# Kernel tuning notes

Hardware: AMD Instinct MI355X
Metric: run time of the kernel (lower is better)

The kernel has to match this reference:

```python
import jax, jax.numpy as jnp
from jax import lax
import numpy as np

# Model hyperparameters (match init_kwargs)
NUM_STEPS = 6
N_ETYPES = 8
D_IN = 128
D_OUT = 128
B, N, E = 32, 1024, 262144  # graphs, nodes per graph, total edges


def setup_inputs() -> dict:
    key = jax.random.key(0)
    ks = jax.random.split(key, 24)
    s = 0.05  # param scale for numeric stability over 6 GRU steps
    inp = {
        "h": jax.random.normal(ks[0], (B, N, D_IN), jnp.float32),
        "src": jax.random.randint(ks[1], (E,), 0, B * N, jnp.int32),
        "dst": jax.random.randint(ks[2], (E,), 0, B * N, jnp.int32),
        "etype": jax.random.randint(ks[3], (E,), 0, N_ETYPES, jnp.int32),
        "W_msg": jax.random.normal(ks[4], (N_ETYPES, D_OUT, D_OUT), jnp.float32) * s,
        "b_msg": jax.random.normal(ks[5], (N_ETYPES, D_OUT), jnp.float32) * s,
        "w_ih": jax.random.normal(ks[6], (3 * D_OUT, D_OUT), jnp.float32) * s,
        "w_hh": jax.random.normal(ks[7], (3 * D_OUT, D_OUT), jnp.float32) * s,
        "b_ih": jax.random.normal(ks[8], (3 * D_OUT,), jnp.float32) * s,
        "b_hh": jax.random.normal(ks[9], (3 * D_OUT,), jnp.float32) * s,
        "conv1_w": jax.random.normal(ks[10], (D_OUT, D_OUT, 3), jnp.float32) * s,
        "conv1_b": jax.random.normal(ks[11], (D_OUT,), jnp.float32) * s,
        "conv2_w": jax.random.normal(ks[12], (D_OUT, D_OUT, 1), jnp.float32) * s,
        "conv2_b": jax.random.normal(ks[13], (D_OUT,), jnp.float32) * s,
        "cc1_w": jax.random.normal(ks[14], (D_IN + D_OUT, D_IN + D_OUT, 3), jnp.float32) * s,
        "cc1_b": jax.random.normal(ks[15], (D_IN + D_OUT,), jnp.float32) * s,
        "cc2_w": jax.random.normal(ks[16], (D_IN + D_OUT, D_IN + D_OUT, 1), jnp.float32) * s,
        "cc2_b": jax.random.normal(ks[17], (D_IN + D_OUT,), jnp.float32) * s,
        "mlp_y_w": jax.random.normal(ks[18], (1, D_OUT), jnp.float32) * s,
        "mlp_y_b": jax.random.normal(ks[19], (1,), jnp.float32) * s,
        "mlp_z_w": jax.random.normal(ks[20], (1, D_IN + D_OUT), jnp.float32) * s,
        "mlp_z_b": jax.random.normal(ks[21], (1,), jnp.float32) * s,
    }
    return inp


def _conv1d(x, w, b):
    # x: [B, C_in, L], w: [C_out, C_in, K]
    y = lax.conv_general_dilated(x, w, (1,), "VALID",
                                 dimension_numbers=("NCW", "OIW", "NCW"))
    return y + b[None, :, None]


def _maxpool1d(x, k, stride):
    return lax.reduce_window(x, -jnp.inf, lax.max,
                             (1, 1, k), (1, 1, stride), "VALID")


def _ggnn(h0, src, dst, etype, W_msg, b_msg, w_ih, w_hh, b_ih, b_hh):
    # h0: [BN, D_OUT] (in_feats == out_feats so no zero-padding needed)
    n_nodes = h0.shape[0]

    def step(h, _):
        # transform each node by every etype weight: [BN, T, O]
        t = jnp.einsum("nd,tod->nto", h, W_msg) + b_msg
        m = t[src, etype]                                   # [E, O] gather
        a = jax.ops.segment_sum(m, dst, num_segments=n_nodes)  # scatter-add
        # torch.nn.GRUCell(a, h)
        gi = a @ w_ih.T + b_ih
        gh = h @ w_hh.T + b_hh
        i_r, i_z, i_n = jnp.split(gi, 3, axis=-1)
        h_r, h_z, h_n = jnp.split(gh, 3, axis=-1)
        r = jax.nn.sigmoid(i_r + h_r)
        z = jax.nn.sigmoid(i_z + h_z)
        n = jnp.tanh(i_n + r * h_n)
        return (1.0 - z) * n + z * h, None

    h_final, _ = lax.scan(step, h0, None, length=NUM_STEPS)
    return h_final


def reference(h, src, dst, etype, W_msg, b_msg, w_ih, w_hh, b_ih, b_hh,
              conv1_w, conv1_b, conv2_w, conv2_b, cc1_w, cc1_b, cc2_w, cc2_b,
              mlp_y_w, mlp_y_b, mlp_z_w, mlp_z_b):
    b, n, d = h.shape
    x = h.reshape(b * n, d)
    h_next = _ggnn(x, src, dst, etype, W_msg, b_msg, w_ih, w_hh, b_ih, b_hh)
    h_i = h_next.reshape(b, n, -1)                   # [B, N, O]
    c_i = jnp.concatenate([h_i, h], axis=-1)          # [B, N, O+D]

    Y_1 = _maxpool1d(jax.nn.relu(_conv1d(h_i.transpose(0, 2, 1), conv1_w, conv1_b)), 3, 2)
    Y_2 = _maxpool1d(jax.nn.relu(_conv1d(Y_1, conv2_w, conv2_b)), 2, 2).transpose(0, 2, 1)
    Z_1 = _maxpool1d(jax.nn.relu(_conv1d(c_i.transpose(0, 2, 1), cc1_w, cc1_b)), 3, 2)
    Z_2 = _maxpool1d(jax.nn.relu(_conv1d(Z_1, cc2_w, cc2_b)), 2, 2).transpose(0, 2, 1)

    before_avg = (Y_2 @ mlp_y_w.T + mlp_y_b) * (Z_2 @ mlp_z_w.T + mlp_z_b)  # [B, L, 1]
    avg = before_avg.mean(axis=1)                     # [B, 1]
    return jax.nn.sigmoid(avg).squeeze(-1)            # [B]
```

## Files before the change

kernel.cpp:

```cpp
#include <hip/hip_runtime.h>
#include <math.h>

#define BB 32
#define NNODE 1024
#define BN 32768
#define NE 262144
#define DD 128
#define NT 8
#define NSTEPS 6
#define NBIN 16
#define SORT_CAP (NE + 2048)
#define NTILES_F 2064
#define M_CAP (NE + 2048)

typedef __attribute__((ext_vector_type(8))) short bf16x8;
typedef __attribute__((ext_vector_type(4))) float f32x4;

static __device__ __forceinline__ float4 ld4(const float* p) { return *(const float4*)p; }
static __device__ __forceinline__ float sigmoidf_(float x) { return 1.f / (1.f + expf(-x)); }
static __device__ __forceinline__ unsigned f2b(float f) {
    unsigned u = __float_as_uint(f);
    return (u + 0x7FFFu + ((u >> 16) & 1u)) >> 16;
}
static __device__ __forceinline__ float b2f(unsigned short b) {
    return __uint_as_float(((unsigned)b) << 16);
}
static __device__ __forceinline__ unsigned pk(float a, float b) {
    return f2b(a) | (f2b(b) << 16);
}
static __device__ __forceinline__ unsigned bmax2(unsigned a, unsigned b) {
    unsigned ah = a & 0xFFFF0000u, bh = b & 0xFFFF0000u;
    unsigned al = a & 0x0000FFFFu, bl = b & 0x0000FFFFu;
    return (ah > bh ? ah : bh) | (al > bl ? al : bl);
}
static __device__ __forceinline__ uint4 bmax4(uint4 a, uint4 b) {
    return make_uint4(bmax2(a.x, b.x), bmax2(a.y, b.y), bmax2(a.z, b.z), bmax2(a.w, b.w));
}

static constexpr size_t OFF_HCUR = 0;
static constexpr size_t OFF_HBF  = OFF_HCUR + (size_t)BN * DD * 4;
static constexpr size_t OFF_CNT  = OFF_HBF  + (size_t)BN * DD * 2;
static constexpr size_t OFF_DOFF = OFF_CNT  + (size_t)BN * NT * 4;
static constexpr size_t OFF_DBLK = OFF_DOFF + (size_t)BN * 4;
static constexpr size_t OFF_HB   = OFF_DBLK + 512;
static constexpr size_t OFF_SSRC = OFF_HB   + 256;
static constexpr size_t OFF_SDST = OFF_SSRC + (size_t)SORT_CAP * 4;
static constexpr size_t OFF_SQ   = OFF_SDST + (size_t)SORT_CAP * 4;
static constexpr size_t OFF_DCUR = OFF_SQ   + (size_t)SORT_CAP * 4;
static constexpr size_t OFF_DEG  = OFF_DCUR + (size_t)BN * 4;
static constexpr size_t OFF_WMB  = OFF_DEG  + (size_t)BN * 4;
static constexpr size_t OFF_WIHB = OFF_WMB  + (size_t)NT * DD * DD * 2;
static constexpr size_t OFF_WHHB = OFF_WIHB + (size_t)3 * DD * DD * 2;
static constexpr size_t OFF_W1PY = OFF_WHHB + (size_t)3 * DD * DD * 2;
static constexpr size_t OFF_W1PZ = OFF_W1PY + (size_t)3 * 128 * 128 * 2;
static constexpr size_t OFF_W2YB = OFF_W1PZ + (size_t)3 * 256 * 256 * 2;
static constexpr size_t OFF_W2ZB = OFF_W2YB + (size_t)128 * 128 * 2;
static constexpr size_t OFF_ABF  = OFF_W2ZB + (size_t)256 * 256 * 2;
static constexpr size_t OFF_H0BF = OFF_ABF  + (size_t)BN * DD * 2;
static constexpr size_t OFF_UN   = OFF_H0BF + (size_t)BN * DD * 2;
static constexpr size_t OFF_M    = OFF_UN;
static constexpr size_t OFF_U1Y  = OFF_UN;
static constexpr size_t OFF_U1Z  = OFF_U1Y + (size_t)32 * 1024 * 128 * 2;
static constexpr size_t OFF_QY   = OFF_U1Z + (size_t)32 * 1024 * 256 * 2;
static constexpr size_t OFF_QZ   = OFF_QY  + (size_t)32 * 255 * 128 * 4;
static constexpr size_t CONV_SZ  = (size_t)32 * 1024 * 128 * 2 + (size_t)32 * 1024 * 256 * 2
                                 + (size_t)32 * 255 * 128 * 4 + (size_t)32 * 255 * 256 * 4;
static constexpr size_t M_SZ     = (size_t)M_CAP * 128 * 2;
static constexpr size_t UN_SZ    = (M_SZ > CONV_SZ ? M_SZ : CONV_SZ);
static constexpr size_t WS_NEED  = OFF_UN + UN_SZ;

#define PREP_BLOCKS 6133
__global__ void k_prep(const float* __restrict__ h_in, float* __restrict__ hcur,
                       unsigned short* __restrict__ hbf, unsigned short* __restrict__ h0bf,
                       const float* __restrict__ Wmsg, unsigned short* __restrict__ wmb,
                       const float* __restrict__ wih, unsigned short* __restrict__ wihb,
                       const float* __restrict__ whh, unsigned short* __restrict__ whhb,
                       const float* __restrict__ c2w, unsigned short* __restrict__ w2yb,
                       const float* __restrict__ z2w, unsigned short* __restrict__ w2zb,
                       const float* __restrict__ c1w, unsigned short* __restrict__ w1py,
                       const float* __restrict__ z1w, unsigned short* __restrict__ w1pz,
                       int* __restrict__ cnt, int* __restrict__ hb,
                       int* __restrict__ ssrc, int* __restrict__ sdst)
{
    int blk = blockIdx.x, tid = threadIdx.x;
    if (blk < 4096) {
        int i = blk * 256 + tid;
        float4 v = ((const float4*)h_in)[i];
        ((float4*)hcur)[i] = v;
        uint2 p = make_uint2(pk(v.x, v.y), pk(v.z, v.w));
        ((uint2*)hbf)[i] = p;
        ((uint2*)h0bf)[i] = p;
    } else if (blk < 4224) {
        int i = (blk - 4096) * 256 + tid;
        float4 v = ((const float4*)Wmsg)[i];
        ((uint2*)wmb)[i] = make_uint2(pk(v.x, v.y), pk(v.z, v.w));
    } else if (blk < 4272) {
        int i = (blk - 4224) * 256 + tid;
        float4 v = ((const float4*)wih)[i];
        ((uint2*)wihb)[i] = make_uint2(pk(v.x, v.y), pk(v.z, v.w));
    } else if (blk < 4320) {
        int i = (blk - 4272) * 256 + tid;
        float4 v = ((const float4*)whh)[i];
        ((uint2*)whhb)[i] = make_uint2(pk(v.x, v.y), pk(v.z, v.w));
    } else if (blk < 4336) {
        int i = (blk - 4320) * 256 + tid;
        float4 v = ((const float4*)c2w)[i];
        ((uint2*)w2yb)[i] = make_uint2(pk(v.x, v.y), pk(v.z, v.w));
    } else if (blk < 4400) {
        int i = (blk - 4336) * 256 + tid;
        float4 v = ((const float4*)z2w)[i];
        ((uint2*)w2zb)[i] = make_uint2(pk(v.x, v.y), pk(v.z, v.w));
    } else if (blk < 4592) {
        int g = (blk - 4400) * 256 + tid;
        int k = g >> 14, rem = g & 16383;
        w1py[g] = (unsigned short)f2b(c1w[(size_t)rem * 3 + k]);
    } else if (blk < 5360) {
        int g = (blk - 4592) * 256 + tid;
        int k = g >> 16, rem = g & 65535;
        w1pz[g] = (unsigned short)f2b(z1w[(size_t)rem * 3 + k]);
    } else if (blk < 5616) {
        ((uint4*)cnt)[(blk - 5360) * 256 + tid] = make_uint4(0, 0, 0, 0);
    } else if (blk < 5617) {
        if (tid < 64) hb[tid] = 0;
    } else if (blk < 5875) {
        ((uint4*)ssrc)[(blk - 5617) * 256 + tid] = make_uint4(0, 0, 0, 0);
    } else {
        ((uint4*)sdst)[(blk - 5875) * 256 + tid] = make_uint4(~0u, ~0u, ~0u, ~0u);
    }
}


__global__ void k_hist(const int* __restrict__ et, const int* __restrict__ dst,
                       int* __restrict__ hb, int* __restrict__ cnt)
{
    __shared__ int lh[NBIN];
    int tid = threadIdx.x;
    if (tid < NBIN) lh[tid] = 0;
    __syncthreads();
    int base = blockIdx.x * 1024;
    for (int k = 0; k < 4; ++k) {
        int e = base + tid + k * 256;
        int t = et[e], d = dst[e];
        atomicAdd(&lh[((d >> 14) << 3) | t], 1);
        atomicAdd(&cnt[d * NT + t], 1);
    }
    __syncthreads();
    if (tid < NBIN) atomicAdd(&hb[tid], lh[tid]);
}

__global__ void k_degA(const int* __restrict__ cnt, int* __restrict__ deg,
                       int* __restrict__ doff, int* __restrict__ dblk)
{
    __shared__ int ps[256];
    int tid = threadIdx.x;
    int v = blockIdx.x * 256 + tid;
    const int* cv = cnt + (size_t)v * NT;
    int d = 0;
#pragma unroll
    for (int t = 0; t < NT; ++t) d += cv[t];
    deg[v] = d;
    ps[tid] = d;
    __syncthreads();
    for (int off = 1; off < 256; off <<= 1) {
        int x = 0;
        if (tid >= off) x = ps[tid - off];
        __syncthreads();
        ps[tid] += x;
        __syncthreads();
    }
    doff[v] = ps[tid] - d;
    if (tid == 255) dblk[blockIdx.x] = ps[255];
}

__global__ void k_scan2(int* __restrict__ hb, int* __restrict__ dblk)
{
    __shared__ int s[128];
    int tid = threadIdx.x;
    s[tid] = dblk[tid];
    __syncthreads();
    if (tid == 0) {
        int acc = 0;
        for (int t = 0; t < NBIN; ++t) {
            hb[16 + t] = acc;
            hb[33 + t] = acc;
            acc += ((hb[t] + 127) >> 7) << 7;
        }
        hb[32] = acc;
        int run = 0;
        for (int i = 0; i < 128; ++i) {
            int x = s[i]; s[i] = run; run += x;
        }
    }
    __syncthreads();
    dblk[tid] = s[tid];
}

__global__ void k_degB(int* __restrict__ doff, int* __restrict__ dcur,
                       const int* __restrict__ dblk)
{
    int v = blockIdx.x * 256 + threadIdx.x;
    int o = doff[v] + dblk[blockIdx.x];
    doff[v] = o;
    dcur[v] = o;
}

__global__ void k_scatter(const int* __restrict__ src, const int* __restrict__ dst,
                          const int* __restrict__ et, int* __restrict__ hb,
                          int* __restrict__ dcur,
                          int* __restrict__ ssrc, int* __restrict__ sdst, int* __restrict__ sq)
{
    __shared__ int lc[NBIN], lbase[NBIN];
    int tid = threadIdx.x;
    if (tid < NBIN) lc[tid] = 0;
    __syncthreads();
    int base = blockIdx.x * 1024;
    int myk[4], myr[4];
    for (int k = 0; k < 4; ++k) {
        int e = base + tid * 4 + k;
        int kk = ((dst[e] >> 14) << 3) | et[e];
        myk[k] = kk;
        myr[k] = atomicAdd(&lc[kk], 1);
    }
    __syncthreads();
    if (tid < NBIN) lbase[tid] = atomicAdd(&hb[33 + tid], lc[tid]);
    __syncthreads();
    for (int k = 0; k < 4; ++k) {
        int e = base + tid * 4 + k;
        int p = lbase[myk[k]] + myr[k];
        int d = dst[e];
        ssrc[p] = src[e];
        sdst[p] = d;
        sq[p] = atomicAdd(&dcur[d], 1);
    }
}


__launch_bounds__(256, 3)
__global__ void k_msg(const int* __restrict__ ssrc, const int* __restrict__ sdst,
                      const int* __restrict__ sq, const int* __restrict__ hb,
                      const unsigned short* __restrict__ hbf,
                      const unsigned short* __restrict__ wmb,
                      unsigned short* __restrict__ m)
{
    __shared__ __align__(16) unsigned short As[128 * 64];
    __shared__ __align__(16) unsigned short Ws[128 * 64];
    __shared__ int sdl[128], ssl[128], sql[128];
    int base = blockIdx.x * 128;
    if (base >= hb[32]) return;
    int bin = 0;
#pragma unroll
    for (int i = 1; i < NBIN; ++i) if (base >= hb[16 + i]) bin = i;
    int t = bin & 7;
    int tid = threadIdx.x;
    if (tid < 128) { sdl[tid] = sdst[base + tid]; ssl[tid] = ssrc[base + tid]; sql[tid] = sq[base + tid]; }
    __syncthreads();
    int lane = tid & 63, wvv = tid >> 6;
    int wm = (wvv >> 1) * 64, wn = (wvv & 1) * 64;
    int lr = lane & 15, lk = lane >> 4;
    f32x4 acc[4][4];
#pragma unroll
    for (int i = 0; i < 4; ++i)
#pragma unroll
        for (int j = 0; j < 4; ++j) acc[i][j] = (f32x4){0.f, 0.f, 0.f, 0.f};

    int r = tid >> 1, halfc = tid & 1;
    unsigned boff = r * 128 + halfc * 64;
    unsigned sw = (r & 7) << 4;
    for (int c0 = 0; c0 < DD; c0 += 64) {
        if (c0) __syncthreads();
        {
            const uint4* hp = (const uint4*)(hbf + (size_t)ssl[r] * DD + c0 + halfc * 32);
            const uint4* wp = (const uint4*)(wmb + (size_t)t * DD * DD + (size_t)r * DD + c0 + halfc * 32);
#pragma unroll
            for (int c = 0; c < 4; ++c) {
                unsigned byte = (boff + c * 16) ^ sw;
                *(uint4*)((char*)As + byte) = hp[c];
                *(uint4*)((char*)Ws + byte) = wp[c];
            }
        }
        __syncthreads();
#pragma unroll
        for (int kc = 0; kc < 2; ++kc) {
            int cb = kc * 64 + lk * 16;
            bf16x8 af[4], bfv[4];
#pragma unroll
            for (int mi = 0; mi < 4; ++mi) {
                int row = wm + mi * 16 + lr;
                af[mi] = *(const bf16x8*)((const char*)As + ((row * 128 + cb) ^ ((row & 7) << 4)));
            }
#pragma unroll
            for (int ni = 0; ni < 4; ++ni) {
                int row = wn + ni * 16 + lr;
                bfv[ni] = *(const bf16x8*)((const char*)Ws + ((row * 128 + cb) ^ ((row & 7) << 4)));
            }
#pragma unroll
            for (int mi = 0; mi < 4; ++mi)
#pragma unroll
                for (int ni = 0; ni < 4; ++ni)
                    acc[mi][ni] = __builtin_amdgcn_mfma_f32_16x16x32_bf16(af[mi], bfv[ni], acc[mi][ni], 0, 0, 0);
        }
    }
    __syncthreads();
    {
        unsigned short* tgt = wn ? Ws : As;
#pragma unroll
        for (int mi = 0; mi < 4; ++mi)
#pragma unroll
            for (int ni = 0; ni < 4; ++ni)
#pragma unroll
                for (int rg = 0; rg < 4; ++rg) {
                    int er = wm + mi * 16 + lk * 4 + rg;
                    int col = (wn + ni * 16 + lr) & 63;
                    unsigned byte = ((unsigned)(er * 128 + col * 2)) ^ ((er & 7) << 4);
                    *(unsigned short*)((char*)tgt + byte) = (unsigned short)f2b(acc[mi][ni][rg]);
                }
    }
    __syncthreads();
    int orow = tid >> 4, ochunk = tid & 15;
#pragma unroll
    for (int p = 0; p < 8; ++p) {
        int row = p * 16 + orow;
        if (sdl[row] >= 0) {
            const char* srcb = (ochunk < 8) ? (const char*)As : (const char*)Ws;
            unsigned byte = ((unsigned)(row * 128 + (ochunk & 7) * 16)) ^ ((row & 7) << 4);
            uint4 v = *(const uint4*)(srcb + byte);
            *(uint4*)(m + (size_t)sql[row] * 128 + ochunk * 8) = v;
        }
    }
}


__launch_bounds__(256)
__global__ void k_agg(const unsigned short* __restrict__ m, const int* __restrict__ deg,
                      const int* __restrict__ doff, const int* __restrict__ cnt,
                      const float* __restrict__ bmsg, unsigned short* __restrict__ abf)
{
    __shared__ float bm[NT * DD];
    int tid = threadIdx.x;
    *(float4*)&bm[tid * 4] = ld4(bmsg + tid * 4);
    __syncthreads();
    int wv = tid >> 6, lane = tid & 63;
    int v = blockIdx.x * 4 + wv;
    int lh = lane >> 5;
    int lc = lane & 31;
    float a0 = 0.f, a1 = 0.f, a2 = 0.f, a3 = 0.f;
    if (lh == 0) {
        const int* cv = cnt + (size_t)v * NT;
        int c0 = lc * 4;
#pragma unroll
        for (int t = 0; t < NT; ++t) {
            float c = (float)cv[t];
            a0 += c * bm[t * DD + c0];
            a1 += c * bm[t * DD + c0 + 1];
            a2 += c * bm[t * DD + c0 + 2];
            a3 += c * bm[t * DD + c0 + 3];
        }
    }
    int d = deg[v], off = doff[v];
    const uint2* mr = (const uint2*)m;
    int npair = d >> 1;
    for (int i = 0; i < npair; ++i) {
        uint2 w = mr[(size_t)(off + 2 * i + lh) * 32 + lc];
        a0 += b2f((unsigned short)(w.x & 0xFFFF));
        a1 += b2f((unsigned short)(w.x >> 16));
        a2 += b2f((unsigned short)(w.y & 0xFFFF));
        a3 += b2f((unsigned short)(w.y >> 16));
    }
    if ((d & 1) && lh == 0) {
        uint2 w = mr[(size_t)(off + d - 1) * 32 + lc];
        a0 += b2f((unsigned short)(w.x & 0xFFFF));
        a1 += b2f((unsigned short)(w.x >> 16));
        a2 += b2f((unsigned short)(w.y & 0xFFFF));
        a3 += b2f((unsigned short)(w.y >> 16));
    }
    a0 += __shfl_xor(a0, 32);
    a1 += __shfl_xor(a1, 32);
    a2 += __shfl_xor(a2, 32);
    a3 += __shfl_xor(a3, 32);
    if (lh == 0)
        ((uint2*)abf)[(size_t)v * 32 + lc] = make_uint2(pk(a0, a1), pk(a2, a3));
}


__launch_bounds__(512, 2)
__global__ void k_gru(const unsigned short* __restrict__ abf, float* __restrict__ h,
                      unsigned short* __restrict__ hbf,
                      const unsigned short* __restrict__ wihb, const unsigned short* __restrict__ whhb,
                      const float* __restrict__ bih, const float* __restrict__ bhh)
{
    __shared__ __align__(16) unsigned short Xs[128 * 128];
    __shared__ __align__(16) unsigned short Ws2[128 * 128];
    int m0 = blockIdx.x * 128;
    int tid = threadIdx.x;
    int lane = tid & 63, wv = tid >> 6;
    int wm = (wv >> 1) * 32, wn = (wv & 1) * 64;
    int lr = lane & 15, lk = lane >> 4;
    f32x4 aR[2][4], aZ[2][4], aI[2][4], aH[2][4];
#pragma unroll
    for (int i = 0; i < 2; ++i)
#pragma unroll
        for (int j = 0; j < 4; ++j) {
            aR[i][j] = (f32x4){0.f, 0.f, 0.f, 0.f};
            aZ[i][j] = (f32x4){0.f, 0.f, 0.f, 0.f};
            aI[i][j] = (f32x4){0.f, 0.f, 0.f, 0.f};
            aH[i][j] = (f32x4){0.f, 0.f, 0.f, 0.f};
        }
    int rx = tid >> 2, qx = tid & 3;
    unsigned bx = rx * 256 + qx * 64, swx = (rx & 7) << 4;
#pragma unroll
    for (int pass = 0; pass < 2; ++pass) {
        const unsigned short* X = pass ? hbf : abf;
        const unsigned short* W = pass ? whhb : wihb;
#pragma unroll
        for (int g = 0; g < 3; ++g) {
            __syncthreads();
            if (g == 0) {
                const uint4* sp = (const uint4*)(X + (size_t)(m0 + rx) * DD + qx * 32);
#pragma unroll
                for (int c = 0; c < 4; ++c)
                    *(uint4*)((char*)Xs + ((bx + c * 16) ^ swx)) = sp[c];
            }
            {
                const uint4* wp = (const uint4*)(W + (size_t)(g * DD + rx) * DD + qx * 32);
#pragma unroll
                for (int c = 0; c < 4; ++c)
                    *(uint4*)((char*)Ws2 + ((bx + c * 16) ^ swx)) = wp[c];
            }
            __syncthreads();
#pragma unroll
            for (int kc = 0; kc < 4; ++kc) {
                int cb = kc * 64 + lk * 16;
                bf16x8 af[2], bfv[4];
#pragma unroll
                for (int mi = 0; mi < 2; ++mi) {
                    int row = wm + mi * 16 + lr;
                    af[mi] = *(const bf16x8*)((const char*)Xs + ((row * 256 + cb) ^ ((row & 7) << 4)));
                }
#pragma unroll
                for (int ni = 0; ni < 4; ++ni) {
                    int row = wn + ni * 16 + lr;
                    bfv[ni] = *(const bf16x8*)((const char*)Ws2 + ((row * 256 + cb) ^ ((row & 7) << 4)));
                }
#pragma unroll
                for (int mi = 0; mi < 2; ++mi)
#pragma unroll
                    for (int ni = 0; ni < 4; ++ni) {
                        if (g == 0)
                            aR[mi][ni] = __builtin_amdgcn_mfma_f32_16x16x32_bf16(af[mi], bfv[ni], aR[mi][ni], 0, 0, 0);
                        else if (g == 1)
                            aZ[mi][ni] = __builtin_amdgcn_mfma_f32_16x16x32_bf16(af[mi], bfv[ni], aZ[mi][ni], 0, 0, 0);
                        else if (pass == 0)
                            aI[mi][ni] = __builtin_amdgcn_mfma_f32_16x16x32_bf16(af[mi], bfv[ni], aI[mi][ni], 0, 0, 0);
                        else
                            aH[mi][ni] = __builtin_amdgcn_mfma_f32_16x16x32_bf16(af[mi], bfv[ni], aH[mi][ni], 0, 0, 0);
                    }
            }
        }
    }
#pragma unroll
    for (int ni = 0; ni < 4; ++ni) {
        int col = wn + ni * 16 + lr;
        float br_ = bih[col] + bhh[col];
        float bz_ = bih[DD + col] + bhh[DD + col];
        float bin_ = bih[2 * DD + col], bhn_ = bhh[2 * DD + col];
#pragma unroll
        for (int mi = 0; mi < 2; ++mi)
#pragma unroll
            for (int rg = 0; rg < 4; ++rg) {
                int v = m0 + wm + mi * 16 + lk * 4 + rg;
                float rr = sigmoidf_(aR[mi][ni][rg] + br_);
                float zz = sigmoidf_(aZ[mi][ni][rg] + bz_);
                float nn = tanhf(aI[mi][ni][rg] + bin_ + rr * (aH[mi][ni][rg] + bhn_));
                float hold = h[(size_t)v * DD + col];
                float hnew = (1.f - zz) * nn + zz * hold;
                h[(size_t)v * DD + col] = hnew;
                hbf[(size_t)v * DD + col] = (unsigned short)f2b(hnew);
            }
    }
}


template <int CIN>
__launch_bounds__(256, 2)
__global__ void k_conv1m(const unsigned short* __restrict__ hbf, const unsigned short* __restrict__ h0bf,
                         const unsigned short* __restrict__ w1p, const float* __restrict__ bias,
                         unsigned short* __restrict__ U1)
{
    __shared__ __align__(16) unsigned short As[128 * 64];
    __shared__ __align__(16) unsigned short Ws[128 * 64];
    int p0 = blockIdx.x * 128, b = blockIdx.y, n0 = blockIdx.z * 128;
    int tid = threadIdx.x;
    int lane = tid & 63, wv = tid >> 6;
    int wm = (wv >> 1) * 64, wn = (wv & 1) * 64;
    int lr = lane & 15, lk = lane >> 4;
    f32x4 acc[4][4];
#pragma unroll
    for (int i = 0; i < 4; ++i)
#pragma unroll
        for (int j = 0; j < 4; ++j) acc[i][j] = (f32x4){0.f, 0.f, 0.f, 0.f};

    int r = tid >> 1, halfc = tid & 1;
    unsigned boff = r * 128 + halfc * 64;
    unsigned sw = (r & 7) << 4;
#pragma unroll
    for (int k = 0; k < 3; ++k) {
        for (int c0 = 0; c0 < CIN; c0 += 64) {
            __syncthreads();
            {
                int row = p0 + k + r; if (row > NNODE - 1) row = NNODE - 1;
                int ci = c0 + halfc * 32;
                const unsigned short* srcp = (CIN == 128 || ci < 128)
                    ? hbf  + ((size_t)(b * NNODE + row)) * DD + ci
                    : h0bf + ((size_t)(b * NNODE + row)) * DD + (ci - 128);
                const uint4* sp = (const uint4*)srcp;
#pragma unroll
                for (int c = 0; c < 4; ++c)
                    *(uint4*)((char*)As + ((boff + c * 16) ^ sw)) = sp[c];
            }
            {
                const uint4* wp = (const uint4*)(w1p + ((size_t)k * CIN + n0 + r) * CIN + c0 + halfc * 32);
#pragma unroll
                for (int c = 0; c < 4; ++c)
                    *(uint4*)((char*)Ws + ((boff + c * 16) ^ sw)) = wp[c];
            }
            __syncthreads();
#pragma unroll
            for (int kc = 0; kc < 2; ++kc) {
                int cb = kc * 64 + lk * 16;
                bf16x8 af[4], bfv[4];
#pragma unroll
                for (int mi = 0; mi < 4; ++mi) {
                    int row = wm + mi * 16 + lr;
                    af[mi] = *(const bf16x8*)((const char*)As + ((row * 128 + cb) ^ ((row & 7) << 4)));
                }
#pragma unroll
                for (int ni = 0; ni < 4; ++ni) {
                    int row = wn + ni * 16 + lr;
                    bfv[ni] = *(const bf16x8*)((const char*)Ws + ((row * 128 + cb) ^ ((row & 7) << 4)));
                }
#pragma unroll
                for (int mi = 0; mi < 4; ++mi)
#pragma unroll
                    for (int ni = 0; ni < 4; ++ni)
                        acc[mi][ni] = __builtin_amdgcn_mfma_f32_16x16x32_bf16(af[mi], bfv[ni], acc[mi][ni], 0, 0, 0);
            }
        }
    }
#pragma unroll
    for (int ni = 0; ni < 4; ++ni) {
        int co = n0 + wn + ni * 16 + lr;
        float bs = bias[co];
#pragma unroll
        for (int mi = 0; mi < 4; ++mi)
#pragma unroll
            for (int rg = 0; rg < 4; ++rg) {
                int pos = p0 + wm + mi * 16 + lk * 4 + rg;
                if (pos < NNODE - 2) {
                    float v = fmaxf(0.f, acc[mi][ni][rg] + bs);
                    U1[((size_t)b * NNODE + pos) * CIN + co] = (unsigned short)f2b(v);
                }
            }
    }
}


template <int CIN>
__launch_bounds__(256, 2)
__global__ void k_conv2m(const unsigned short* __restrict__ U1, const unsigned short* __restrict__ w2b,
                         const float* __restrict__ bias, float* __restrict__ Q)
{
    __shared__ __align__(16) unsigned short As[128 * 64];
    __shared__ __align__(16) unsigned short Ws[128 * 64];
    int m0 = blockIdx.x * 128, b = blockIdx.y, n0 = blockIdx.z * 128;
    int tid = threadIdx.x;
    int lane = tid & 63, wv = tid >> 6;
    int wm = (wv >> 1) * 64, wn = (wv & 1) * 64;
    int lr = lane & 15, lk = lane >> 4;
    f32x4 acc[4][4];
#pragma unroll
    for (int i = 0; i < 4; ++i)
#pragma unroll
        for (int j = 0; j < 4; ++j) acc[i][j] = (f32x4){0.f, 0.f, 0.f, 0.f};

    int r = tid >> 1, halfc = tid & 1;
    unsigned boff = r * 128 + halfc * 64;
    unsigned sw = (r & 7) << 4;
    for (int c0 = 0; c0 < CIN; c0 += 64) {
        __syncthreads();
        {
            int pr = 2 * (m0 + r);
            int r0 = pr, r1 = pr + 1, r2v = pr + 2;
            if (r2v > NNODE - 1) r2v = NNODE - 1;
            if (r1 > NNODE - 1) r1 = NNODE - 1;
            int ci = c0 + halfc * 32;
            const unsigned short* bp = U1 + (size_t)b * NNODE * CIN + ci;
            const uint4* p0q = (const uint4*)(bp + (size_t)r0 * CIN);
            const uint4* p1q = (const uint4*)(bp + (size_t)r1 * CIN);
            const uint4* p2q = (const uint4*)(bp + (size_t)r2v * CIN);
#pragma unroll
            for (int c = 0; c < 4; ++c) {
                uint4 mm = bmax4(bmax4(p0q[c], p1q[c]), p2q[c]);
                *(uint4*)((char*)As + ((boff + c * 16) ^ sw)) = mm;
            }
        }
        {
            const uint4* wp = (const uint4*)(w2b + (size_t)(n0 + r) * CIN + c0 + halfc * 32);
#pragma unroll
            for (int c = 0; c < 4; ++c)
                *(uint4*)((char*)Ws + ((boff + c * 16) ^ sw)) = wp[c];
        }
        __syncthreads();
#pragma unroll
        for (int kc = 0; kc < 2; ++kc) {
            int cb = kc * 64 + lk * 16;
            bf16x8 af[4], bfv[4];
#pragma unroll
            for (int mi = 0; mi < 4; ++mi) {
                int row = wm + mi * 16 + lr;
                af[mi] = *(const bf16x8*)((const char*)As + ((row * 128 + cb) ^ ((row & 7) << 4)));
            }
#pragma unroll
            for (int ni = 0; ni < 4; ++ni) {
                int row = wn + ni * 16 + lr;
                bfv[ni] = *(const bf16x8*)((const char*)Ws + ((row * 128 + cb) ^ ((row & 7) << 4)));
            }
#pragma unroll
            for (int mi = 0; mi < 4; ++mi)
#pragma unroll
                for (int ni = 0; ni < 4; ++ni)
                    acc[mi][ni] = __builtin_amdgcn_mfma_f32_16x16x32_bf16(af[mi], bfv[ni], acc[mi][ni], 0, 0, 0);
        }
    }
#pragma unroll
    for (int ni = 0; ni < 4; ++ni) {
        int co = n0 + wn + ni * 16 + lr;
        float bs = bias[co];
#pragma unroll
        for (int mi = 0; mi < 4; ++mi) {
            int l0 = m0 + wm + mi * 16 + lk * 4;
            float v0 = fmaxf(0.f, acc[mi][ni][0] + bs);
            float v1 = fmaxf(0.f, acc[mi][ni][1] + bs);
            float v2 = fmaxf(0.f, acc[mi][ni][2] + bs);
            float v3 = fmaxf(0.f, acc[mi][ni][3] + bs);
            int jq = l0 >> 1;
            if (jq < 255)     Q[((size_t)b * 255 + jq) * CIN + co]     = fmaxf(v0, v1);
            if (jq + 1 < 255) Q[((size_t)b * 255 + jq + 1) * CIN + co] = fmaxf(v2, v3);
        }
    }
}


__launch_bounds__(256)
__global__ void k_final(const float* __restrict__ QY, const float* __restrict__ QZ,
                        const float* __restrict__ wy, const float* __restrict__ by,
                        const float* __restrict__ wz, const float* __restrict__ bz,
                        float* __restrict__ out)
{
    int b = blockIdx.x, tid = threadIdx.x;
    float p = 0.f;
    if (tid < 255) {
        const float* qy = QY + ((size_t)(b * 255 + tid)) * 128;
        const float* qz = QZ + ((size_t)(b * 255 + tid)) * 256;
        float dy = 0.f, dz = 0.f;
        for (int c = 0; c < 128; c += 4) {
            float4 q = ld4(qy + c), wv = ld4(wy + c);
            dy += q.x * wv.x + q.y * wv.y + q.z * wv.z + q.w * wv.w;
        }
        for (int c = 0; c < 256; c += 4) {
            float4 q = ld4(qz + c), wv = ld4(wz + c);
            dz += q.x * wv.x + q.y * wv.y + q.z * wv.z + q.w * wv.w;
        }
        p = (dy + by[0]) * (dz + bz[0]);
    }
    __shared__ float red[4];
    for (int off = 32; off > 0; off >>= 1) p += __shfl_down(p, off);
    if ((tid & 63) == 0) red[tid >> 6] = p;
    __syncthreads();
    if (tid == 0) {
        float s = red[0] + red[1] + red[2] + red[3];
        out[b] = 1.f / (1.f + expf(-s / 255.f));
    }
}


extern "C" void kernel_launch(void* const* d_in, const int* in_sizes, int n_in,
                              void* d_out, int out_size, void* d_ws, size_t ws_size,
                              hipStream_t stream)
{
    const float* h_in = (const float*)d_in[0];
    const int* src = (const int*)d_in[1];
    const int* dst = (const int*)d_in[2];
    const int* et  = (const int*)d_in[3];
    const float* Wmsg = (const float*)d_in[4];
    const float* bmsg = (const float*)d_in[5];
    const float* wih = (const float*)d_in[6];
    const float* whh = (const float*)d_in[7];
    const float* bih = (const float*)d_in[8];
    const float* bhh = (const float*)d_in[9];
    const float* c1w = (const float*)d_in[10];
    const float* c1b = (const float*)d_in[11];
    const float* c2w = (const float*)d_in[12];
    const float* c2b = (const float*)d_in[13];
    const float* z1w = (const float*)d_in[14];
    const float* z1b = (const float*)d_in[15];
    const float* z2w = (const float*)d_in[16];
    const float* z2b = (const float*)d_in[17];
    const float* wy  = (const float*)d_in[18];
    const float* by  = (const float*)d_in[19];
    const float* wz  = (const float*)d_in[20];
    const float* bz  = (const float*)d_in[21];
    float* out = (float*)d_out;

    if (ws_size < WS_NEED) return;

    char* ws = (char*)d_ws;
    float* hcur = (float*)(ws + OFF_HCUR);
    unsigned short* hbf  = (unsigned short*)(ws + OFF_HBF);
    int*   cnt  = (int*)(ws + OFF_CNT);
    int*   doff = (int*)(ws + OFF_DOFF);
    int*   dblk = (int*)(ws + OFF_DBLK);
    int*   hb   = (int*)(ws + OFF_HB);
    int*   ssrc = (int*)(ws + OFF_SSRC);
    int*   sdst = (int*)(ws + OFF_SDST);
    int*   sq   = (int*)(ws + OFF_SQ);
    int*   dcur = (int*)(ws + OFF_DCUR);
    int*   deg  = (int*)(ws + OFF_DEG);
    unsigned short* wmb  = (unsigned short*)(ws + OFF_WMB);
    unsigned short* wihb = (unsigned short*)(ws + OFF_WIHB);
    unsigned short* whhb = (unsigned short*)(ws + OFF_WHHB);
    unsigned short* w1py = (unsigned short*)(ws + OFF_W1PY);
    unsigned short* w1pz = (unsigned short*)(ws + OFF_W1PZ);
    unsigned short* w2yb = (unsigned short*)(ws + OFF_W2YB);
    unsigned short* w2zb = (unsigned short*)(ws + OFF_W2ZB);
    unsigned short* abf  = (unsigned short*)(ws + OFF_ABF);
    unsigned short* h0bf = (unsigned short*)(ws + OFF_H0BF);
    unsigned short* mbuf = (unsigned short*)(ws + OFF_M);
    unsigned short* U1Y  = (unsigned short*)(ws + OFF_U1Y);
    unsigned short* U1Z  = (unsigned short*)(ws + OFF_U1Z);
    float* QY   = (float*)(ws + OFF_QY);
    float* QZ   = (float*)(ws + OFF_QZ);

    k_prep<<<PREP_BLOCKS, 256, 0, stream>>>(h_in, hcur, hbf, h0bf, Wmsg, wmb, wih, wihb, whh, whhb,
                                            c2w, w2yb, z2w, w2zb, c1w, w1py, z1w, w1pz,
                                            cnt, hb, ssrc, sdst);

    k_hist<<<256, 256, 0, stream>>>(et, dst, hb, cnt);
    k_degA<<<128, 256, 0, stream>>>(cnt, deg, doff, dblk);
    k_scan2<<<1, 128, 0, stream>>>(hb, dblk);
    k_degB<<<128, 256, 0, stream>>>(doff, dcur, dblk);
    k_scatter<<<256, 256, 0, stream>>>(src, dst, et, hb, dcur, ssrc, sdst, sq);

    for (int s = 0; s < NSTEPS; ++s) {
        k_msg<<<NTILES_F, 256, 0, stream>>>(ssrc, sdst, sq, hb, hbf, wmb, mbuf);
        k_agg<<<BN / 4, 256, 0, stream>>>(mbuf, deg, doff, cnt, bmsg, abf);
        k_gru<<<BN / 128, 512, 0, stream>>>(abf, hcur, hbf, wihb, whhb, bih, bhh);
    }

    k_conv1m<128><<<dim3(8, 32, 1), 256, 0, stream>>>(hbf, h0bf, w1py, c1b, U1Y);
    k_conv2m<128><<<dim3(4, 32, 1), 256, 0, stream>>>(U1Y, w2yb, c2b, QY);
    k_conv1m<256><<<dim3(8, 32, 2), 256, 0, stream>>>(hbf, h0bf, w1pz, z1b, U1Z);
    k_conv2m<256><<<dim3(4, 32, 2), 256, 0, stream>>>(U1Z, w2zb, z2b, QZ);
    k_final<<<32, 256, 0, stream>>>(QY, QZ, wy, by, wz, bz, out);
}
```

Baseline: 558.1 us.

## Fuse message aggregation into GRU kernel and raise k_msg occupancy bound

```diff
diff --git a/kernel.cpp b/kernel.cpp
--- a/kernel.cpp
+++ b/kernel.cpp
@@ -35,6 +35,16 @@
 }
 static __device__ __forceinline__ uint4 bmax4(uint4 a, uint4 b) {
     return make_uint4(bmax2(a.x, b.x), bmax2(a.y, b.y), bmax2(a.z, b.z), bmax2(a.w, b.w));
+}
+static __device__ __forceinline__ void upacc(float* ac, uint4 w0, uint4 w1) {
+    ac[0] += b2f((unsigned short)(w0.x & 0xFFFF)); ac[1] += b2f((unsigned short)(w0.x >> 16));
+    ac[2] += b2f((unsigned short)(w0.y & 0xFFFF)); ac[3] += b2f((unsigned short)(w0.y >> 16));
+    ac[4] += b2f((unsigned short)(w0.z & 0xFFFF)); ac[5] += b2f((unsigned short)(w0.z >> 16));
+    ac[6] += b2f((unsigned short)(w0.w & 0xFFFF)); ac[7] += b2f((unsigned short)(w0.w >> 16));
+    ac[8] += b2f((unsigned short)(w1.x & 0xFFFF)); ac[9] += b2f((unsigned short)(w1.x >> 16));
+    ac[10] += b2f((unsigned short)(w1.y & 0xFFFF)); ac[11] += b2f((unsigned short)(w1.y >> 16));
+    ac[12] += b2f((unsigned short)(w1.z & 0xFFFF)); ac[13] += b2f((unsigned short)(w1.z >> 16));
+    ac[14] += b2f((unsigned short)(w1.w & 0xFFFF)); ac[15] += b2f((unsigned short)(w1.w >> 16));
 }
 
 static constexpr size_t OFF_HCUR = 0;
@@ -235,7 +245,7 @@
 }
 
 
-__launch_bounds__(256, 3)
+__launch_bounds__(256, 4)
 __global__ void k_msg(const int* __restrict__ ssrc, const int* __restrict__ sdst,
                       const int* __restrict__ sq, const int* __restrict__ hb,
                       const unsigned short* __restrict__ hbf,
@@ -330,68 +340,55 @@
 }
 
 
-__launch_bounds__(256)
-__global__ void k_agg(const unsigned short* __restrict__ m, const int* __restrict__ deg,
-                      const int* __restrict__ doff, const int* __restrict__ cnt,
-                      const float* __restrict__ bmsg, unsigned short* __restrict__ abf)
-{
-    __shared__ float bm[NT * DD];
+__launch_bounds__(512, 2)
+__global__ void k_gruagg(const unsigned short* __restrict__ m, const int* __restrict__ deg,
+                         const int* __restrict__ doff, const int* __restrict__ cnt,
+                         const float* __restrict__ bmsg,
+                         float* __restrict__ h, unsigned short* __restrict__ hbf,
+                         const unsigned short* __restrict__ wihb, const unsigned short* __restrict__ whhb,
+                         const float* __restrict__ bih, const float* __restrict__ bhh)
+{
+    __shared__ __align__(16) unsigned short Xs[128 * 128];
+    __shared__ __align__(16) unsigned short Ws2[128 * 128];
+    __shared__ float bmS[NT * DD];
+    int m0 = blockIdx.x * 128;
     int tid = threadIdx.x;
-    *(float4*)&bm[tid * 4] = ld4(bmsg + tid * 4);
-    __syncthreads();
-    int wv = tid >> 6, lane = tid & 63;
-    int v = blockIdx.x * 4 + wv;
-    int lh = lane >> 5;
-    int lc = lane & 31;
-    float a0 = 0.f, a1 = 0.f, a2 = 0.f, a3 = 0.f;
-    if (lh == 0) {
-        const int* cv = cnt + (size_t)v * NT;
-        int c0 = lc * 4;
+    ((float2*)bmS)[tid] = ((const float2*)bmsg)[tid];
+
+    int rx = tid >> 2, qx = tid & 3;
+    unsigned bx = rx * 256 + qx * 64, swx = (rx & 7) << 4;
+    int v = m0 + rx;
+    int d = deg[v], off = doff[v];
+    int cv[NT];
+    {
+        uint4 c0 = *(const uint4*)(cnt + (size_t)v * NT);
+        uint4 c1 = *(const uint4*)(cnt + (size_t)v * NT + 4);
+        cv[0] = c0.x; cv[1] = c0.y; cv[2] = c0.z; cv[3] = c0.w;
+        cv[4] = c1.x; cv[5] = c1.y; cv[6] = c1.z; cv[7] = c1.w;
+    }
+    __syncthreads();
+#pragma unroll
+    for (int half = 0; half < 2; ++half) {
+        float ac[16];
+#pragma unroll
+        for (int j = 0; j < 16; ++j) ac[j] = 0.f;
 #pragma unroll
         for (int t = 0; t < NT; ++t) {
             float c = (float)cv[t];
-            a0 += c * bm[t * DD + c0];
-            a1 += c * bm[t * DD + c0 + 1];
-            a2 += c * bm[t * DD + c0 + 2];
-            a3 += c * bm[t * DD + c0 + 3];
-        }
-    }
-    int d = deg[v], off = doff[v];
-    const uint2* mr = (const uint2*)m;
-    int npair = d >> 1;
-    for (int i = 0; i < npair; ++i) {
-        uint2 w = mr[(size_t)(off + 2 * i + lh) * 32 + lc];
-        a0 += b2f((unsigned short)(w.x & 0xFFFF));
-        a1 += b2f((unsigned short)(w.x >> 16));
-        a2 += b2f((unsigned short)(w.y & 0xFFFF));
-        a3 += b2f((unsigned short)(w.y >> 16));
-    }
-    if ((d & 1) && lh == 0) {
-        uint2 w = mr[(size_t)(off + d - 1) * 32 + lc];
-        a0 += b2f((unsigned short)(w.x & 0xFFFF));
-        a1 += b2f((unsigned short)(w.x >> 16));
-        a2 += b2f((unsigned short)(w.y & 0xFFFF));
-        a3 += b2f((unsigned short)(w.y >> 16));
-    }
-    a0 += __shfl_xor(a0, 32);
-    a1 += __shfl_xor(a1, 32);
-    a2 += __shfl_xor(a2, 32);
-    a3 += __shfl_xor(a3, 32);
-    if (lh == 0)
-        ((uint2*)abf)[(size_t)v * 32 + lc] = make_uint2(pk(a0, a1), pk(a2, a3));
-}
-
-
-__launch_bounds__(512, 2)
-__global__ void k_gru(const unsigned short* __restrict__ abf, float* __restrict__ h,
-                      unsigned short* __restrict__ hbf,
-                      const unsigned short* __restrict__ wihb, const unsigned short* __restrict__ whhb,
-                      const float* __restrict__ bih, const float* __restrict__ bhh)
-{
-    __shared__ __align__(16) unsigned short Xs[128 * 128];
-    __shared__ __align__(16) unsigned short Ws2[128 * 128];
-    int m0 = blockIdx.x * 128;
-    int tid = threadIdx.x;
+            const float* bp = &bmS[t * DD + qx * 32 + half * 16];
+#pragma unroll
+            for (int j = 0; j < 16; ++j) ac[j] += c * bp[j];
+        }
+        for (int e = 0; e < d; ++e) {
+            const uint4* pp = (const uint4*)(m + ((size_t)(off + e)) * DD + qx * 32 + half * 16);
+            upacc(ac, pp[0], pp[1]);
+        }
+        uint4 o0 = make_uint4(pk(ac[0], ac[1]), pk(ac[2], ac[3]), pk(ac[4], ac[5]), pk(ac[6], ac[7]));
+        uint4 o1 = make_uint4(pk(ac[8], ac[9]), pk(ac[10], ac[11]), pk(ac[12], ac[13]), pk(ac[14], ac[15]));
+        *(uint4*)((char*)Xs + ((bx + half * 32) ^ swx)) = o0;
+        *(uint4*)((char*)Xs + ((bx + half * 32 + 16) ^ swx)) = o1;
+    }
+
     int lane = tid & 63, wv = tid >> 6;
     int wm = (wv >> 1) * 32, wn = (wv & 1) * 64;
     int lr = lane & 15, lk = lane >> 4;
@@ -405,17 +402,14 @@
             aI[i][j] = (f32x4){0.f, 0.f, 0.f, 0.f};
             aH[i][j] = (f32x4){0.f, 0.f, 0.f, 0.f};
         }
-    int rx = tid >> 2, qx = tid & 3;
-    unsigned bx = rx * 256 + qx * 64, swx = (rx & 7) << 4;
 #pragma unroll
     for (int pass = 0; pass < 2; ++pass) {
-        const unsigned short* X = pass ? hbf : abf;
         const unsigned short* W = pass ? whhb : wihb;
 #pragma unroll
         for (int g = 0; g < 3; ++g) {
             __syncthreads();
-            if (g == 0) {
-                const uint4* sp = (const uint4*)(X + (size_t)(m0 + rx) * DD + qx * 32);
+            if (g == 0 && pass == 1) {
+                const uint4* sp = (const uint4*)(hbf + (size_t)(m0 + rx) * DD + qx * 32);
 #pragma unroll
                 for (int c = 0; c < 4; ++c)
                     *(uint4*)((char*)Xs + ((bx + c * 16) ^ swx)) = sp[c];
@@ -467,14 +461,14 @@
         for (int mi = 0; mi < 2; ++mi)
 #pragma unroll
             for (int rg = 0; rg < 4; ++rg) {
-                int v = m0 + wm + mi * 16 + lk * 4 + rg;
+                int vv = m0 + wm + mi * 16 + lk * 4 + rg;
                 float rr = sigmoidf_(aR[mi][ni][rg] + br_);
                 float zz = sigmoidf_(aZ[mi][ni][rg] + bz_);
                 float nn = tanhf(aI[mi][ni][rg] + bin_ + rr * (aH[mi][ni][rg] + bhn_));
-                float hold = h[(size_t)v * DD + col];
+                float hold = h[(size_t)vv * DD + col];
                 float hnew = (1.f - zz) * nn + zz * hold;
-                h[(size_t)v * DD + col] = hnew;
-                hbf[(size_t)v * DD + col] = (unsigned short)f2b(hnew);
+                h[(size_t)vv * DD + col] = hnew;
+                hbf[(size_t)vv * DD + col] = (unsigned short)f2b(hnew);
             }
     }
 }
@@ -732,7 +726,6 @@
     unsigned short* w1pz = (unsigned short*)(ws + OFF_W1PZ);
     unsigned short* w2yb = (unsigned short*)(ws + OFF_W2YB);
     unsigned short* w2zb = (unsigned short*)(ws + OFF_W2ZB);
-    unsigned short* abf  = (unsigned short*)(ws + OFF_ABF);
     unsigned short* h0bf = (unsigned short*)(ws + OFF_H0BF);
     unsigned short* mbuf = (unsigned short*)(ws + OFF_M);
     unsigned short* U1Y  = (unsigned short*)(ws + OFF_U1Y);
@@ -752,8 +745,8 @@
 
     for (int s = 0; s < NSTEPS; ++s) {
         k_msg<<<NTILES_F, 256, 0, stream>>>(ssrc, sdst, sq, hb, hbf, wmb, mbuf);
-        k_agg<<<BN / 4, 256, 0, stream>>>(mbuf, deg, doff, cnt, bmsg, abf);
-        k_gru<<<BN / 128, 512, 0, stream>>>(abf, hcur, hbf, wihb, whhb, bih, bhh);
+        k_gruagg<<<BN / 128, 512, 0, stream>>>(mbuf, deg, doff, cnt, bmsg,
+                                               hcur, hbf, wihb, whhb, bih, bhh);
     }
 
     k_conv1m<128><<<dim3(8, 32, 1), 256, 0, stream>>>(hbf, h0bf, w1py, c1b, U1Y);
```

Result: no change. 565.7 us (+1.4%).
